# Performance work log

Hardware: AMD Instinct MI355X
Metric: run time of the kernel (lower is better)

## Reference

```python
import jax, jax.numpy as jnp
import numpy as np

NUM_LEVELS = 4
RADIUS = 4


def _bilinear_zeros(img, x, y):
    """Bilinear sample img (N,H,W) at absolute pixel coords x,y (N,S,S),
    zeros padding outside, matching torch grid_sample(align_corners=True,
    padding_mode='zeros') with absolute->normalized->absolute roundtrip."""
    N, H, W = img.shape
    x0 = jnp.floor(x); y0 = jnp.floor(y)
    x1 = x0 + 1.0;     y1 = y0 + 1.0
    wx1 = x - x0; wx0 = 1.0 - wx1
    wy1 = y - y0; wy0 = 1.0 - wy1
    flat = img.reshape(N, H * W)

    def gather(xi, yi):
        valid = (xi >= 0) & (xi <= W - 1) & (yi >= 0) & (yi <= H - 1)
        xc = jnp.clip(xi, 0, W - 1).astype(jnp.int32)
        yc = jnp.clip(yi, 0, H - 1).astype(jnp.int32)
        idx = (yc * W + xc).reshape(N, -1)
        v = jnp.take_along_axis(flat, idx, axis=1).reshape(xi.shape)
        return jnp.where(valid, v, jnp.zeros((), img.dtype))

    return (wy0 * wx0 * gather(x0, y0) + wy0 * wx1 * gather(x1, y0)
            + wy1 * wx0 * gather(x0, y1) + wy1 * wx1 * gather(x1, y1))


def _avg_pool2(v):
    N, H, W = v.shape
    return v.reshape(N, H // 2, 2, W // 2, 2).mean(axis=(2, 4))


def setup_inputs() -> dict:
    key = jax.random.key(0)
    k1, k2, k3 = jax.random.split(key, 3)
    B, M, C, H, W = 2, 4096, 256, 64, 64
    fmap1 = jax.random.normal(k1, (B, M, C), dtype=jnp.float32)
    fmap2 = jax.random.normal(k2, (B, C, H, W), dtype=jnp.float32)
    u = jax.random.uniform(k3, (B, M, 2), dtype=jnp.float32)
    centroids_coords = u * jnp.array([W - 1, H - 1], dtype=jnp.float32)
    return {"fmap1": fmap1, "fmap2": fmap2, "centroids_coords": centroids_coords}


def reference(fmap1, fmap2, centroids_coords):
    B, M, C = fmap1.shape
    _, _, H, W = fmap2.shape
    side = 2 * RADIUS + 1

    # correlation volume: (B, M, H, W) -> (B*M, H, W)
    corr = jnp.einsum('bmc,bchw->bmhw', fmap1, fmap2).reshape(B * M, H, W)

    d = jnp.arange(-RADIUS, RADIUS + 1, dtype=centroids_coords.dtype)
    di, dj = jnp.meshgrid(d, d, indexing='ij')
    delta = jnp.stack([di, dj], axis=-1)  # (S, S, 2): ch0 = x-offset, ch1 = y-offset

    c = centroids_coords.reshape(B * M, 1, 1, 2)
    vol = corr
    feats = []
    for lvl in range(NUM_LEVELS):
        sc = c + delta                        # (B*M, S, S, 2)
        sampled = _bilinear_zeros(vol, sc[..., 0], sc[..., 1])
        feats.append(sampled.reshape(B, M, side * side))
        c = c / 2.0
        if lvl < NUM_LEVELS - 1:
            vol = _avg_pool2(vol)
    # (B, M, num_levels*S*S) -> (B, out_channels, M)
    return jnp.concatenate(feats, axis=-1).transpose(0, 2, 1)
```

## Files before the change

### kernel.cpp

```cpp
#include <hip/hip_runtime.h>
#include <stdint.h>
#include <stddef.h>

static constexpr int Bb = 2;
static constexpr int Mq = 4096;
static constexpr int Cc = 256;
static constexpr int Hh = 64, Ww = 64;
static constexpr int Np = Hh * Ww;
static constexpr int RAD = 4;
static constexpr int SIDE = 2 * RAD + 1;
static constexpr int KPL = SIDE * SIDE;
static constexpr int NLVL = 4;
static constexpr int KTOT = NLVL * KPL;

static constexpr size_t L1BUF_B  = 0;
static constexpr size_t WINBUF_B = (size_t)Bb * Mq * 1024 * 2;
static constexpr size_t ABF_B    = WINBUF_B + (size_t)Bb * Mq * 100 * 4;
static constexpr size_t BT_B     = ABF_B + (size_t)Bb * Mq * Cc * 2;

typedef float floatx4 __attribute__((ext_vector_type(4)));
typedef short shortx8 __attribute__((ext_vector_type(8)));

union BfPack {
    shortx8 v;
    unsigned short u[8];
};

__device__ __forceinline__ unsigned short f2bf(float f) {
    unsigned int x = __float_as_uint(f);
    x += 0x7fffu + ((x >> 16) & 1u);
    return (unsigned short)(x >> 16);
}

__device__ __forceinline__ float bf2f(unsigned short u) {
    return __uint_as_float((unsigned int)u << 16);
}

__device__ __forceinline__ void gll16(const void* g, void* l) {
    __builtin_amdgcn_global_load_lds(
        (const __attribute__((address_space(1))) unsigned int*)g,
        (__attribute__((address_space(3))) unsigned int*)l, 16, 0, 0);
}

__global__ __launch_bounds__(256)
void cvt_kernel(const float* __restrict__ f1, const float* __restrict__ f2,
                unsigned short* __restrict__ Abf, unsigned short* __restrict__ Bt)
{
    __shared__ float tile[64 * 65];
    const int tid = threadIdx.x;
    if (blockIdx.x < 1024) {
        const int t = blockIdx.x * 256 + tid;
        const float4 v0 = *(const float4*)(f1 + (size_t)t * 8);
        const float4 v1 = *(const float4*)(f1 + (size_t)t * 8 + 4);
        BfPack p;
        p.u[0] = f2bf(v0.x); p.u[1] = f2bf(v0.y);
        p.u[2] = f2bf(v0.z); p.u[3] = f2bf(v0.w);
        p.u[4] = f2bf(v1.x); p.u[5] = f2bf(v1.y);
        p.u[6] = f2bf(v1.z); p.u[7] = f2bf(v1.w);
        *(shortx8*)(Abf + (size_t)t * 8) = p.v;
        return;
    }
    const int bid = blockIdx.x - 1024;
    const int p0 = (bid & 63) * 64;
    const int c0 = ((bid >> 6) & 3) * 64;
    const int b  = bid >> 8;

    const int pl = tid & 63;
    const int cb = tid >> 6;
#pragma unroll
    for (int it = 0; it < 16; ++it) {
        const int cl = it * 4 + cb;
        tile[cl * 65 + pl] = f2[((size_t)(b * Cc + c0 + cl)) * Np + p0 + pl];
    }
    __syncthreads();

    const int cg = (tid & 7) * 8;
#pragma unroll
    for (int it = 0; it < 2; ++it) {
        const int pw = it * 32 + (tid >> 3);
        BfPack p;
#pragma unroll
        for (int u = 0; u < 8; ++u)
            p.u[u] = f2bf(tile[(cg + u) * 65 + pw]);
        *(shortx8*)(Bt + ((size_t)(b * Np + p0 + pw)) * Cc + c0 + cg) = p.v;
    }
}

__global__ __launch_bounds__(256)
void corr_gemm_pool_kernel(const unsigned short* __restrict__ Abf,
                           const unsigned short* __restrict__ Bt,
                           const float* __restrict__ cent,
                           unsigned short* __restrict__ l1buf,
                           float* __restrict__ winbuf)
{
    __shared__ union {
        unsigned short stage[2][2][128 * 32];
        float corrT[32 * 131];
    } sm;
    __shared__ int qx0s[128], qy0s[128];

    const int b    = blockIdx.z;
    const int bm0  = blockIdx.y * 128;
    const int bx   = blockIdx.x;
    const int bn0  = bx * 128;
    const int tid  = threadIdx.x;
    const int lane = tid & 63;
    const int wave = tid >> 6;
    const int lane15 = lane & 15;
    const int quad   = lane >> 4;
    const int wm = (wave >> 1) * 64;
    const int wn = (wave & 1) * 64;

    if (tid < 128) {
        const float cx = cent[(size_t)(b * Mq + bm0 + tid) * 2 + 0];
        const float cy = cent[(size_t)(b * Mq + bm0 + tid) * 2 + 1];
        qx0s[tid] = (int)floorf(cx) - RAD;
        qy0s[tid] = (int)floorf(cy) - RAD;
    }

    const int lrow = lane >> 2;
    const int lkg  = (((lane & 3) ^ ((lrow >> 1) & 3))) * 8;
    const unsigned short* aptr = Abf + (size_t)(b * Mq + bm0 + wave * 16 + lrow) * Cc + lkg;
    const unsigned short* bptr = Bt  + (size_t)(b * Np + bn0 + wave * 16 + lrow) * Cc + lkg;

    floatx4 acc[4][4];
#pragma unroll
    for (int i = 0; i < 4; ++i)
#pragma unroll
        for (int j = 0; j < 4; ++j)
            acc[i][j] = floatx4{0.0f, 0.0f, 0.0f, 0.0f};

    gll16(aptr,           &sm.stage[0][0][wave * 512]);
    gll16(aptr + 64 * Cc, &sm.stage[0][0][2048 + wave * 512]);
    gll16(bptr,           &sm.stage[0][1][wave * 512]);
    gll16(bptr + 64 * Cc, &sm.stage[0][1][2048 + wave * 512]);

    const int rq = (quad ^ ((lane15 >> 1) & 3)) * 8;

    for (int k0 = 0; k0 < 8; ++k0) {
        __syncthreads();
        if (k0 < 7) {
            const int nb = (k0 + 1) & 1;
            const int ko = (k0 + 1) * 32;
            gll16(aptr + ko,           &sm.stage[nb][0][wave * 512]);
            gll16(aptr + 64 * Cc + ko, &sm.stage[nb][0][2048 + wave * 512]);
            gll16(bptr + ko,           &sm.stage[nb][1][wave * 512]);
            gll16(bptr + 64 * Cc + ko, &sm.stage[nb][1][2048 + wave * 512]);
        }
        const unsigned short* la = sm.stage[k0 & 1][0];
        const unsigned short* lb = sm.stage[k0 & 1][1];
        shortx8 af[4], bf[4];
#pragma unroll
        for (int i = 0; i < 4; ++i)
            af[i] = *(const shortx8*)&la[(wm + i * 16 + lane15) * 32 + rq];
#pragma unroll
        for (int j = 0; j < 4; ++j)
            bf[j] = *(const shortx8*)&lb[(wn + j * 16 + lane15) * 32 + rq];
#pragma unroll
        for (int i = 0; i < 4; ++i)
#pragma unroll
            for (int j = 0; j < 4; ++j)
                acc[i][j] = __builtin_amdgcn_mfma_f32_16x16x32_bf16(
                    af[i], bf[j], acc[i][j], 0, 0, 0);
    }

    float* corrT = sm.corrT;
    const int m_local = tid >> 3;
    const int xi      = tid & 7;
#pragma unroll
    for (int c = 0; c < 4; ++c) {
        __syncthreads();
        if ((wave >> 1) == (c >> 1)) {
#pragma unroll
            for (int ii = 0; ii < 2; ++ii) {
                const int i = 2 * (c & 1) + ii;
#pragma unroll
                for (int j = 0; j < 4; ++j) {
#pragma unroll
                    for (int reg = 0; reg < 4; ++reg) {
                        const int rl = ii * 16 + quad * 4 + reg;
                        const int n  = wn + j * 16 + lane15;
                        corrT[rl * 131 + n] = acc[i][j][reg];
                    }
                }
            }
        }
        __syncthreads();

        const int mg = 32 * c + m_local;
        const size_t gq = (size_t)(b * Mq + bm0 + mg);
        const float* T = &corrT[m_local * 131];

#pragma unroll
        for (int k = 0; k < 4; ++k) {
            const int c1 = xi + 8 * k;
            const float v = 0.25f * (T[2 * c1] + T[2 * c1 + 1]
                                   + T[64 + 2 * c1] + T[64 + 2 * c1 + 1]);
            l1buf[gq * 1024 + bx * 32 + c1] = f2bf(v);
        }

        const int x0w = qx0s[mg];
        const int y0w = qy0s[mg];
#pragma unroll
        for (int par = 0; par < 2; ++par) {
            const int wy = 2 * bx + par - y0w;
            if (wy >= 0 && wy < 10) {
#pragma unroll
                for (int t = 0; t < 2; ++t) {
                    const int wx = xi + t * 8;
                    if (wx < 10) {
                        const int x = x0w + wx;
                        if (x >= 0 && x < Ww)
                            winbuf[gq * 100 + wy * 10 + wx] = T[par * 64 + x];
                    }
                }
            }
        }
    }
}

__global__ __launch_bounds__(256)
void pyr_sample_kernel(const float* __restrict__ cent,
                       const unsigned short* __restrict__ l1buf,
                       const float* __restrict__ winbuf,
                       float* __restrict__ out)
{
    __shared__ float l1[8][1024];
    __shared__ float l2[8][256];
    __shared__ float l3[8][64];
    __shared__ float win0[8][100];
    __shared__ float qcx[8], qcy[8];
    __shared__ int   qx0[8], qy0[8];

    const int tid = threadIdx.x;
    const int b   = blockIdx.x >> 9;
    const int m0  = (blockIdx.x & 511) * 8;
    const size_t gq0 = (size_t)(b * Mq + m0);

    if (tid < 8) {
        const float cx = cent[(gq0 + tid) * 2 + 0];
        const float cy = cent[(gq0 + tid) * 2 + 1];
        qcx[tid] = cx; qcy[tid] = cy;
        qx0[tid] = (int)floorf(cx) - RAD;
        qy0[tid] = (int)floorf(cy) - RAD;
    }

#pragma unroll
    for (int it = 0; it < 4; ++it) {
        const int v = it * 256 + tid;
        const int q = v >> 7;
        const int o = v & 127;
        BfPack p;
        p.v = *(const shortx8*)&l1buf[(gq0 + q) * 1024 + o * 8];
#pragma unroll
        for (int u = 0; u < 8; ++u)
            l1[q][o * 8 + u] = bf2f(p.u[u]);
    }
    if (tid < 200) {
        const int q = tid / 25;
        const int o = tid - q * 25;
        *(float4*)&win0[q][o * 4] = *(const float4*)&winbuf[(gq0 + q) * 100 + o * 4];
    }
    __syncthreads();

#pragma unroll
    for (int i = 0; i < 8; ++i) {
        const int idx = i * 256 + tid;
        const int q = idx >> 8;
        const int c = idx & 255;
        const int cy2 = c >> 4, cx2 = c & 15;
        const float* s = &l1[q][(2 * cy2) * 32 + 2 * cx2];
        l2[q][c] = 0.25f * (s[0] + s[1] + s[32] + s[33]);
    }
    __syncthreads();
#pragma unroll
    for (int i = 0; i < 2; ++i) {
        const int idx = i * 256 + tid;
        const int q = idx >> 6;
        const int c = idx & 63;
        const int cy3 = c >> 3, cx3 = c & 7;
        const float* s = &l2[q][(2 * cy3) * 16 + 2 * cx3];
        l3[q][c] = 0.25f * (s[0] + s[1] + s[16] + s[17]);
    }
    __syncthreads();

    for (int i = 0; i < 11; ++i) {
        const int idx = i * 256 + tid;
        if (idx >= KTOT * 8) break;
        const int q  = idx & 7;
        const int kk = idx >> 3;
        const int lvl = kk / KPL;
        const int r   = kk - lvl * KPL;
        const int di  = r / SIDE;
        const int dj  = r - di * SIDE;

        const int w = Ww >> lvl;
        const float scale = 1.0f / (float)(1 << lvl);
        const float x = qcx[q] * scale + (float)(di - RAD);
        const float y = qcy[q] * scale + (float)(dj - RAD);

        const float x0f = floorf(x), y0f = floorf(y);
        const float wx1 = x - x0f, wx0 = 1.0f - wx1;
        const float wy1 = y - y0f, wy0 = 1.0f - wy1;
        const float fmx = (float)(w - 1);
        const bool vx0 = (x0f >= 0.0f) && (x0f <= fmx);
        const bool vx1 = (x0f + 1.0f >= 0.0f) && (x0f + 1.0f <= fmx);
        const bool vy0 = (y0f >= 0.0f) && (y0f <= fmx);
        const bool vy1 = (y0f + 1.0f >= 0.0f) && (y0f + 1.0f <= fmx);

        const int ix0 = (int)x0f, iy0 = (int)y0f;

        const float* buf;
        int stride, ox, oy;
        if (lvl == 0)      { buf = win0[q]; stride = 10; ox = qx0[q]; oy = qy0[q]; }
        else if (lvl == 1) { buf = l1[q];   stride = 32; ox = 0; oy = 0; }
        else if (lvl == 2) { buf = l2[q];   stride = 16; ox = 0; oy = 0; }
        else               { buf = l3[q];   stride =  8; ox = 0; oy = 0; }

        const int cx0 = ix0 - ox, cx1 = ix0 + 1 - ox;
        const int cy0r = iy0 - oy, cy1r = iy0 + 1 - oy;
        const float g00 = (vx0 && vy0) ? buf[cy0r * stride + cx0] : 0.0f;
        const float g10 = (vx1 && vy0) ? buf[cy0r * stride + cx1] : 0.0f;
        const float g01 = (vx0 && vy1) ? buf[cy1r * stride + cx0] : 0.0f;
        const float g11 = (vx1 && vy1) ? buf[cy1r * stride + cx1] : 0.0f;

        out[((size_t)b * KTOT + kk) * Mq + m0 + q] =
            wy0 * (wx0 * g00 + wx1 * g10) + wy1 * (wx0 * g01 + wx1 * g11);
    }
}

extern "C" void kernel_launch(void* const* d_in, const int* in_sizes, int n_in,
                              void* d_out, int out_size, void* d_ws, size_t ws_size,
                              hipStream_t stream)
{
    const float* fmap1 = (const float*)d_in[0];
    const float* fmap2 = (const float*)d_in[1];
    const float* cent  = (const float*)d_in[2];
    char* ws = (char*)d_ws;
    unsigned short* l1buf = (unsigned short*)(ws + L1BUF_B);
    float* winbuf = (float*)(ws + WINBUF_B);
    unsigned short* Abf = (unsigned short*)(ws + ABF_B);
    unsigned short* Bt  = (unsigned short*)(ws + BT_B);
    float* out = (float*)d_out;

    cvt_kernel<<<1536, 256, 0, stream>>>(fmap1, fmap2, Abf, Bt);

    dim3 ggrid(Np / 128, Mq / 128, Bb);
    corr_gemm_pool_kernel<<<ggrid, 256, 0, stream>>>(Abf, Bt, cent, l1buf, winbuf);

    const int nblk = Bb * Mq / 8;
    pyr_sample_kernel<<<nblk, 256, 0, stream>>>(cent, l1buf, winbuf, out);
}
```

Baseline: 118.6 us.

## Pool fmap2 before GEMM and compute level-0 windows directly per query

Uses linearity: average-pooling the correlation volume equals correlating against a pooled fmap2. The conversion kernel now also writes a 2x2-pooled bf16 fmap2, and the GEMM runs only against the 1024 pooled pixels instead of 4096. The full-resolution level-0 values are needed only in a 10x10 window per query, so a new wave-per-query kernel computes those dot products directly from bf16 data with shuffle reductions. This removes most of the full-resolution GEMM work. The cost is an extra kernel launch, scattered gathers in the window kernel, and pooling in bf16 before the product, which changes rounding.

```diff
diff --git a/kernel.cpp b/kernel.cpp
--- a/kernel.cpp
+++ b/kernel.cpp
@@ -7,6 +7,7 @@
 static constexpr int Cc = 256;
 static constexpr int Hh = 64, Ww = 64;
 static constexpr int Np = Hh * Ww;
+static constexpr int NL1 = 1024;
 static constexpr int RAD = 4;
 static constexpr int SIDE = 2 * RAD + 1;
 static constexpr int KPL = SIDE * SIDE;
@@ -17,6 +18,7 @@
 static constexpr size_t WINBUF_B = (size_t)Bb * Mq * 1024 * 2;
 static constexpr size_t ABF_B    = WINBUF_B + (size_t)Bb * Mq * 100 * 4;
 static constexpr size_t BT_B     = ABF_B + (size_t)Bb * Mq * Cc * 2;
+static constexpr size_t B1T_B    = BT_B + (size_t)Bb * Np * Cc * 2;
 
 typedef float floatx4 __attribute__((ext_vector_type(4)));
 typedef short shortx8 __attribute__((ext_vector_type(8)));
@@ -44,9 +46,10 @@
 
 __global__ __launch_bounds__(256)
 void cvt_kernel(const float* __restrict__ f1, const float* __restrict__ f2,
-                unsigned short* __restrict__ Abf, unsigned short* __restrict__ Bt)
+                unsigned short* __restrict__ Abf, unsigned short* __restrict__ Bt,
+                unsigned short* __restrict__ B1t)
 {
-    __shared__ float tile[64 * 65];
+    __shared__ float tile[64 * 132];
     const int tid = threadIdx.x;
     if (blockIdx.x < 1024) {
         const int t = blockIdx.x * 256 + tid;
@@ -60,49 +63,135 @@
         *(shortx8*)(Abf + (size_t)t * 8) = p.v;
         return;
     }
-    const int bid = blockIdx.x - 1024;
-    const int p0 = (bid & 63) * 64;
-    const int c0 = ((bid >> 6) & 3) * 64;
-    const int b  = bid >> 8;
-
-    const int pl = tid & 63;
-    const int cb = tid >> 6;
-#pragma unroll
-    for (int it = 0; it < 16; ++it) {
-        const int cl = it * 4 + cb;
-        tile[cl * 65 + pl] = f2[((size_t)(b * Cc + c0 + cl)) * Np + p0 + pl];
+    const int bid  = blockIdx.x - 1024;
+    const int b    = bid >> 7;
+    const int cblk = (bid >> 5) & 3;
+    const int y1   = bid & 31;
+
+#pragma unroll
+    for (int i = 0; i < 8; ++i) {
+        const int v  = i * 256 + tid;
+        const int c  = v >> 5;
+        const int f4 = v & 31;
+        *(float4*)&tile[c * 132 + f4 * 4] =
+            *(const float4*)&f2[((size_t)(b * Cc + cblk * 64 + c)) * Np + y1 * 128 + f4 * 4];
     }
     __syncthreads();
 
-    const int cg = (tid & 7) * 8;
-#pragma unroll
-    for (int it = 0; it < 2; ++it) {
-        const int pw = it * 32 + (tid >> 3);
+#pragma unroll
+    for (int i = 0; i < 4; ++i) {
+        const int w  = i * 256 + tid;
+        const int rp = w >> 3;
+        const int cg = w & 7;
         BfPack p;
 #pragma unroll
         for (int u = 0; u < 8; ++u)
-            p.u[u] = f2bf(tile[(cg + u) * 65 + pw]);
-        *(shortx8*)(Bt + ((size_t)(b * Np + p0 + pw)) * Cc + c0 + cg) = p.v;
+            p.u[u] = f2bf(tile[(cg * 8 + u) * 132 + rp]);
+        *(shortx8*)&Bt[((size_t)(b * Np + y1 * 128 + rp)) * Cc + cblk * 64 + cg * 8] = p.v;
+    }
+
+    {
+        const int x1 = tid >> 3;
+        const int cg = tid & 7;
+        BfPack p;
+#pragma unroll
+        for (int u = 0; u < 8; ++u) {
+            const int c = cg * 8 + u;
+            const float v = 0.25f * (tile[c * 132 + 2 * x1]      + tile[c * 132 + 2 * x1 + 1]
+                                   + tile[c * 132 + 64 + 2 * x1] + tile[c * 132 + 64 + 2 * x1 + 1]);
+            p.u[u] = f2bf(v);
+        }
+        *(shortx8*)&B1t[((size_t)(b * NL1 + y1 * 32 + x1)) * Cc + cblk * 64 + cg * 8] = p.v;
     }
 }
 
 __global__ __launch_bounds__(256)
-void corr_gemm_pool_kernel(const unsigned short* __restrict__ Abf,
-                           const unsigned short* __restrict__ Bt,
-                           const float* __restrict__ cent,
-                           unsigned short* __restrict__ l1buf,
-                           float* __restrict__ winbuf)
+void win_kernel(const unsigned short* __restrict__ Abf,
+                const unsigned short* __restrict__ Bt,
+                const float* __restrict__ cent,
+                float* __restrict__ winbuf)
+{
+    const int tid  = threadIdx.x;
+    const int wave = tid >> 6;
+    const int lane = tid & 63;
+    const int h    = lane >> 5;
+    const int cl   = lane & 31;
+    const size_t gq = (size_t)blockIdx.x * 4 + wave;
+    const int b = (int)(gq >> 12);
+
+    float a[8];
+    {
+        BfPack ap;
+        ap.v = *(const shortx8*)&Abf[gq * Cc + cl * 8];
+#pragma unroll
+        for (int u = 0; u < 8; ++u) a[u] = bf2f(ap.u[u]);
+    }
+
+    const float cx = cent[gq * 2 + 0];
+    const float cy = cent[gq * 2 + 1];
+    const int x0 = (int)floorf(cx) - RAD;
+    const int y0 = (int)floorf(cy) - RAD;
+    const int xlo = x0 > 0 ? x0 : 0;
+    const int xhim = x0 + 9 < Ww - 1 ? x0 + 9 : Ww - 1;
+    const int npx = xhim - xlo + 1;
+    const int wxbase = xlo - x0;
+
+    for (int wy = 0; wy < 10; ++wy) {
+        const int y = y0 + wy;
+        if ((unsigned)y > 63u) continue;
+        const unsigned short* bp =
+            Bt + ((size_t)(b * Np) + (size_t)(y * Ww + xlo)) * Cc + cl * 8;
+
+        float acc0 = 0.f, acc1 = 0.f, acc2 = 0.f, acc3 = 0.f, acc4 = 0.f;
+#pragma unroll
+        for (int it = 0; it < 5; ++it) {
+            const int p = it * 2 + h;
+            if (p < npx) {
+                BfPack bv;
+                bv.v = *(const shortx8*)&bp[p * Cc];
+                float s = 0.f;
+#pragma unroll
+                for (int u = 0; u < 8; ++u)
+                    s = fmaf(a[u], bf2f(bv.u[u]), s);
+                if (it == 0) acc0 += s;
+                else if (it == 1) acc1 += s;
+                else if (it == 2) acc2 += s;
+                else if (it == 3) acc3 += s;
+                else acc4 += s;
+            }
+        }
+#pragma unroll
+        for (int m = 16; m >= 1; m >>= 1) {
+            acc0 += __shfl_xor(acc0, m);
+            acc1 += __shfl_xor(acc1, m);
+            acc2 += __shfl_xor(acc2, m);
+            acc3 += __shfl_xor(acc3, m);
+            acc4 += __shfl_xor(acc4, m);
+        }
+        float val = acc0;
+        val = (cl == 1) ? acc1 : val;
+        val = (cl == 2) ? acc2 : val;
+        val = (cl == 3) ? acc3 : val;
+        val = (cl == 4) ? acc4 : val;
+        const int p = cl * 2 + h;
+        if (cl < 5 && p < npx)
+            winbuf[gq * 100 + wy * 10 + wxbase + p] = val;
+    }
+}
+
+__global__ __launch_bounds__(256)
+void l1_gemm_kernel(const unsigned short* __restrict__ Abf,
+                    const unsigned short* __restrict__ B1t,
+                    unsigned short* __restrict__ l1buf)
 {
     __shared__ union {
         unsigned short stage[2][2][128 * 32];
-        float corrT[32 * 131];
+        float corrT[32 * 132];
     } sm;
-    __shared__ int qx0s[128], qy0s[128];
 
     const int b    = blockIdx.z;
     const int bm0  = blockIdx.y * 128;
-    const int bx   = blockIdx.x;
-    const int bn0  = bx * 128;
+    const int bn0  = blockIdx.x * 128;
     const int tid  = threadIdx.x;
     const int lane = tid & 63;
     const int wave = tid >> 6;
@@ -111,17 +200,10 @@
     const int wm = (wave >> 1) * 64;
     const int wn = (wave & 1) * 64;
 
-    if (tid < 128) {
-        const float cx = cent[(size_t)(b * Mq + bm0 + tid) * 2 + 0];
-        const float cy = cent[(size_t)(b * Mq + bm0 + tid) * 2 + 1];
-        qx0s[tid] = (int)floorf(cx) - RAD;
-        qy0s[tid] = (int)floorf(cy) - RAD;
-    }
-
     const int lrow = lane >> 2;
     const int lkg  = (((lane & 3) ^ ((lrow >> 1) & 3))) * 8;
     const unsigned short* aptr = Abf + (size_t)(b * Mq + bm0 + wave * 16 + lrow) * Cc + lkg;
-    const unsigned short* bptr = Bt  + (size_t)(b * Np + bn0 + wave * 16 + lrow) * Cc + lkg;
+    const unsigned short* bptr = B1t + (size_t)(b * NL1 + bn0 + wave * 16 + lrow) * Cc + lkg;
 
     floatx4 acc[4][4];
 #pragma unroll
@@ -165,8 +247,8 @@
     }
 
     float* corrT = sm.corrT;
-    const int m_local = tid >> 3;
-    const int xi      = tid & 7;
+    const int row = tid >> 3;
+    const int g   = tid & 7;
 #pragma unroll
     for (int c = 0; c < 4; ++c) {
         __syncthreads();
@@ -180,42 +262,23 @@
                     for (int reg = 0; reg < 4; ++reg) {
                         const int rl = ii * 16 + quad * 4 + reg;
                         const int n  = wn + j * 16 + lane15;
-                        corrT[rl * 131 + n] = acc[i][j][reg];
+                        corrT[rl * 132 + n] = acc[i][j][reg];
                     }
                 }
             }
         }
         __syncthreads();
 
-        const int mg = 32 * c + m_local;
-        const size_t gq = (size_t)(b * Mq + bm0 + mg);
-        const float* T = &corrT[m_local * 131];
-
-#pragma unroll
-        for (int k = 0; k < 4; ++k) {
-            const int c1 = xi + 8 * k;
-            const float v = 0.25f * (T[2 * c1] + T[2 * c1 + 1]
-                                   + T[64 + 2 * c1] + T[64 + 2 * c1 + 1]);
-            l1buf[gq * 1024 + bx * 32 + c1] = f2bf(v);
-        }
-
-        const int x0w = qx0s[mg];
-        const int y0w = qy0s[mg];
-#pragma unroll
-        for (int par = 0; par < 2; ++par) {
-            const int wy = 2 * bx + par - y0w;
-            if (wy >= 0 && wy < 10) {
-#pragma unroll
-                for (int t = 0; t < 2; ++t) {
-                    const int wx = xi + t * 8;
-                    if (wx < 10) {
-                        const int x = x0w + wx;
-                        if (x >= 0 && x < Ww)
-                            winbuf[gq * 100 + wy * 10 + wx] = T[par * 64 + x];
-                    }
-                }
-            }
-        }
+        const size_t gq = (size_t)(b * Mq + bm0 + 32 * c + row);
+        const float* T = &corrT[row * 132];
+        BfPack p0, p1;
+#pragma unroll
+        for (int u = 0; u < 8; ++u) {
+            p0.u[u] = f2bf(T[g * 16 + u]);
+            p1.u[u] = f2bf(T[g * 16 + 8 + u]);
+        }
+        *(shortx8*)&l1buf[gq * 1024 + bn0 + g * 16]     = p0.v;
+        *(shortx8*)&l1buf[gq * 1024 + bn0 + g * 16 + 8] = p1.v;
     }
 }
 
@@ -341,12 +404,15 @@
     float* winbuf = (float*)(ws + WINBUF_B);
     unsigned short* Abf = (unsigned short*)(ws + ABF_B);
     unsigned short* Bt  = (unsigned short*)(ws + BT_B);
+    unsigned short* B1t = (unsigned short*)(ws + B1T_B);
     float* out = (float*)d_out;
 
-    cvt_kernel<<<1536, 256, 0, stream>>>(fmap1, fmap2, Abf, Bt);
-
-    dim3 ggrid(Np / 128, Mq / 128, Bb);
-    corr_gemm_pool_kernel<<<ggrid, 256, 0, stream>>>(Abf, Bt, cent, l1buf, winbuf);
+    cvt_kernel<<<1280, 256, 0, stream>>>(fmap1, fmap2, Abf, Bt, B1t);
+
+    win_kernel<<<Bb * Mq / 4, 256, 0, stream>>>(Abf, Bt, cent, winbuf);
+
+    dim3 ggrid(NL1 / 128, Mq / 128, Bb);
+    l1_gemm_kernel<<<ggrid, 256, 0, stream>>>(Abf, B1t, l1buf);
 
     const int nblk = Bb * Mq / 8;
     pyr_sample_kernel<<<nblk, 256, 0, stream>>>(cent, l1buf, winbuf, out);
```

After: 135.4 us. +14.1%, slower.
